# Kernel tuning notes

Measured on AMD Instinct MI355X. Metric: run time of the kernel, lower is better.

## Reference

```python
import jax, jax.numpy as jnp
import numpy as np

# config constants (from init_kwargs config['masking'])
MASK_RATIO = 0.15
SPAN_MIN = 5
SPAN_MAX = 20


def _generate_batch_masks(key, batch_size, seq_len):
    """Span-based random masking, exact-count adjusted. [B, S] bool."""
    target_masked = int(seq_len * MASK_RATIO)              # static
    avg_span = (SPAN_MIN + SPAN_MAX) / 2.0
    n_spans = max(1, int(target_masked / avg_span * 2))    # estimated_spans
    k_len, k_start, k_noise = jax.random.split(key, 3)

    span_lengths = jax.random.randint(k_len, (batch_size, n_spans), SPAN_MIN, SPAN_MAX + 1)
    starts = jax.random.randint(k_start, (batch_size, n_spans), 0, max(1, seq_len - SPAN_MIN))
    ends = jnp.minimum(starts + span_lengths, seq_len)

    # Span coverage via +1/-1 scatter + cumsum (equivalent to the per-span
    # boolean scatter loop in the torch code, fully on-device).
    b_idx = jnp.arange(batch_size)[:, None]
    delta = jnp.zeros((batch_size, seq_len + 1), jnp.int32)
    delta = delta.at[b_idx, starts].add(1).at[b_idx, ends].add(-1)
    coverage = jnp.cumsum(delta[:, :seq_len], axis=1) > 0   # [B, S] bool

    # Exact-count adjustment: equivalent to randomly removing excess masked
    # positions / randomly adding unmasked positions until count == target.
    # Masked positions get score in (1,2), unmasked in (0,1); top-k = keep a
    # random masked subset, fill remainder with random unmasked positions.
    noise = jax.random.uniform(k_noise, (batch_size, seq_len))
    score = coverage.astype(jnp.float32) + noise
    _, top_idx = jax.lax.top_k(score, target_masked)        # [B, target]
    masks = jnp.zeros((batch_size, seq_len), bool).at[b_idx, top_idx].set(True)
    return masks


def setup_inputs() -> dict:
    key = jax.random.key(0)
    k1, k2 = jax.random.split(key)
    features = jax.random.normal(k1, (128, 16384, 6), dtype=jnp.float32)
    mask_token = jax.random.normal(k2, (6,), dtype=jnp.float32) * 0.02
    return {"features": features, "mask_token": mask_token}


def reference(features, mask_token):
    B, S, F = features.shape
    key = jax.random.key(1234)  # plays the role of the module's torch.Generator seed
    masks = _generate_batch_masks(key, B, S)
    # _apply_valid_mask_vectorized: only mask non-NaN positions (channel 0)
    valid = ~jnp.isnan(features[:, :, 0])
    masks = masks & valid
    # apply_mask_to_features: replace masked positions with mask_token
    masked_features = jnp.where(masks[:, :, None], mask_token[None, None, :], features)
    return masked_features
```

## Files before the change

### kernel.cpp

```cpp
#include <hip/hip_runtime.h>
#include <stdint.h>

constexpr int NB = 128;
constexpr int SEQ = 16384;
constexpr int NF = 6;
constexpr int NSPANS = 393;
constexpr uint32_t TGT = 2457u;
constexpr int ROWF = SEQ * NF;
constexpr int ROWF4 = ROWF / 4;
constexpr int TOT4 = NB * ROWF4;

constexpr int FM_OFF = 0;
constexpr int FM_DW = NB * (SEQ / 32);
constexpr size_t WS_BYTES = (size_t)FM_DW * 4;

struct Keys {
  uint32_t klo0, klo1;
  uint32_t khi_s0, khi_s1;
  uint32_t klo_s0, klo_s1;
  uint32_t kn0, kn1;
};

__host__ __device__ inline void tf2x32(uint32_t k0, uint32_t k1,
                                       uint32_t x0, uint32_t x1,
                                       uint32_t& o0, uint32_t& o1) {
  uint32_t ks[3] = {k0, k1, k0 ^ k1 ^ 0x1BD11BDAu};
  uint32_t a = x0 + ks[0], b = x1 + ks[1];
  const uint32_t rot[2][4] = {{13u,15u,26u,6u},{17u,29u,16u,24u}};
#pragma unroll
  for (int i = 0; i < 5; ++i) {
    const uint32_t* r = rot[i & 1];
#pragma unroll
    for (int j = 0; j < 4; ++j) {
      a += b;
      b = (b << r[j]) | (b >> (32u - r[j]));
      b ^= a;
    }
    a += ks[(i + 1) % 3];
    b += ks[(i + 2) % 3] + (uint32_t)(i + 1);
  }
  o0 = a; o1 = b;
}

__device__ inline uint32_t rbits(uint32_t k0, uint32_t k1, uint32_t j) {
  uint32_t o0, o1;
  tf2x32(k0, k1, 0u, j, o0, o1);
  return o0 ^ o1;
}

__global__ __launch_bounds__(1024)
void maskgen_kernel(uint32_t* __restrict__ ws, Keys K) {
  __shared__ uint32_t hist[4096];
  __shared__ uint32_t cov[SEQ / 32];
  __shared__ uint32_t fm[SEQ / 32];
  __shared__ uint32_t wsum[16], ssum[16];
  __shared__ int tielist[256];
  __shared__ uint32_t sH, sA, sT, sN;
  __shared__ int tieCnt;

  const int t = threadIdx.x;
  const int lane = t & 63;
  const int wid = t >> 6;
  const uint32_t b = blockIdx.x;

  for (int i = t; i < 4096; i += 1024) hist[i] = 0u;
  if (t < SEQ / 32) cov[t] = 0u;
  if (t == 0) tieCnt = 0;
  __syncthreads();

  if (t < NSPANS) {
    uint32_t j = b * (uint32_t)NSPANS + (uint32_t)t;
    uint32_t lenb = rbits(K.klo0, K.klo1, j);
    uint32_t len = 5u + (lenb & 15u);
    uint32_t hb = rbits(K.khi_s0, K.khi_s1, j);
    uint32_t lb = rbits(K.klo_s0, K.klo_s1, j);
    const uint32_t span = 16379u;
    uint32_t start = ((hb % span) * 400u + (lb % span)) % span;
    uint32_t end = start + len; if (end > (uint32_t)SEQ) end = SEQ;
    uint32_t w0 = start >> 5, w1 = (end - 1u) >> 5;
    for (uint32_t w = w0; w <= w1; ++w) {
      uint32_t bs = (w == w0) ? (start & 31u) : 0u;
      uint32_t be = (w == w1) ? ((end - 1u) & 31u) : 31u;
      uint32_t n = be - bs + 1u;
      uint32_t m = (n >= 32u) ? 0xFFFFFFFFu : (((1u << n) - 1u) << bs);
      atomicOr(&cov[w], m);
    }
  }
  __syncthreads();

  const uint32_t jb = b << 14;
  uint32_t sr[16];
#pragma unroll
  for (int i = 0; i < 16; ++i) {
    int s = (i << 10) + t;
    uint32_t bits = rbits(K.kn0, K.kn1, jb + (uint32_t)s);
    uint32_t si = (bits >> 9) + (((cov[s >> 5] >> (s & 31)) & 1u) << 23);
    sr[i] = si;
    atomicAdd(&hist[si >> 12], 1u);
  }
  __syncthreads();

  {
    uint32_t mysum = 0;
#pragma unroll
    for (int i = 0; i < 4; ++i) mysum += hist[t * 4 + i];
    uint32_t v = mysum;
#pragma unroll
    for (int off = 1; off < 64; off <<= 1) {
      uint32_t n = __shfl_down(v, off, 64);
      if (lane + off < 64) v += n;
    }
    if (lane == 0) wsum[wid] = v;
    __syncthreads();
    if (t < 16) {
      uint32_t w = wsum[t];
#pragma unroll
      for (int off = 1; off < 16; off <<= 1) {
        uint32_t n = __shfl_down(w, off, 64);
        if (t + off < 16) w += n;
      }
      ssum[t] = w;
    }
    __syncthreads();
    uint32_t mine = v + (ssum[wid] - wsum[wid]);
    uint32_t above = mine - mysum;
    if (above < TGT && TGT <= mine) {
      uint32_t run = above;
      for (int hb = t * 4 + 3; hb >= t * 4; --hb) {
        uint32_t c = hist[hb];
        if (run + c >= TGT) { sH = (uint32_t)hb; sA = run; break; }
        run += c;
      }
    }
  }
  __syncthreads();
  uint32_t H = sH;
  uint32_t targetB = TGT - sA;

  for (int i = t; i < 4096; i += 1024) hist[i] = 0u;
  __syncthreads();

#pragma unroll
  for (int i = 0; i < 16; ++i) {
    uint32_t si = sr[i];
    if ((si >> 12) == H) atomicAdd(&hist[si & 4095u], 1u);
  }
  __syncthreads();
  {
    uint32_t mysum = 0;
#pragma unroll
    for (int i = 0; i < 4; ++i) mysum += hist[t * 4 + i];
    uint32_t v = mysum;
#pragma unroll
    for (int off = 1; off < 64; off <<= 1) {
      uint32_t n = __shfl_down(v, off, 64);
      if (lane + off < 64) v += n;
    }
    if (lane == 0) wsum[wid] = v;
    __syncthreads();
    if (t < 16) {
      uint32_t w = wsum[t];
#pragma unroll
      for (int off = 1; off < 16; off <<= 1) {
        uint32_t n = __shfl_down(w, off, 64);
        if (t + off < 16) w += n;
      }
      ssum[t] = w;
    }
    __syncthreads();
    uint32_t mine = v + (ssum[wid] - wsum[wid]);
    uint32_t above = mine - mysum;
    if (above < targetB && targetB <= mine) {
      uint32_t run = above;
      for (int lb = t * 4 + 3; lb >= t * 4; --lb) {
        uint32_t c = hist[lb];
        if (run + c >= targetB) {
          sT = (H << 12) | (uint32_t)lb;
          sN = targetB - run;
          break;
        }
        run += c;
      }
    }
  }
  __syncthreads();
  uint32_t T = sT, need = sN;

#pragma unroll
  for (int i = 0; i < 16; ++i) {
    int s = (i << 10) + t;
    uint32_t si = sr[i];
    unsigned long long bal = __ballot(si > T);
    if (si == T) {
      int idx = atomicAdd(&tieCnt, 1);
      if (idx < 256) tielist[idx] = s;
    }
    if (lane == 0)       fm[s >> 5] = (uint32_t)bal;
    else if (lane == 32) fm[s >> 5] = (uint32_t)(bal >> 32);
  }
  __syncthreads();
  int tc = tieCnt < 256 ? tieCnt : 256;
  if (t < tc) {
    int s = tielist[t];
    uint32_t rank = 0;
    for (int j = 0; j < tc; ++j) rank += (tielist[j] < s) ? 1u : 0u;
    if (rank < need) atomicOr(&fm[s >> 5], 1u << (s & 31));
  }
  __syncthreads();
  if (t < SEQ / 32) ws[FM_OFF + (b << 9) + t] = fm[t];
}

__global__ __launch_bounds__(256)
void apply3(const float* __restrict__ feat, const float* __restrict__ tok,
            const uint32_t* __restrict__ ws, float* __restrict__ out) {
  __shared__ float4 tile[768];
  const int t = threadIdx.x;
  const uint32_t n = blockIdx.x;
  const float4* f4 = (const float4*)feat + (size_t)n * 768;
  float4* o4 = (float4*)out + (size_t)n * 768;

  tile[t] = f4[t];
  tile[t + 256] = f4[t + 256];
  tile[t + 512] = f4[t + 512];
  uint32_t w = ws[FM_OFF + (n << 4) + (t >> 4)];
  float t0 = tok[0], t1 = tok[1], t2 = tok[2], t3 = tok[3], t4 = tok[4], t5 = tok[5];
  __syncthreads();

  float* lf = (float*)tile + t * 12;
  uint32_t bit0 = (uint32_t)(2 * t) & 31u;
  bool m0 = (w >> bit0) & 1u;
  bool m1 = (w >> (bit0 + 1u)) & 1u;
  m0 = m0 && !(lf[0] != lf[0]);
  m1 = m1 && !(lf[6] != lf[6]);
  if (m0) { lf[0] = t0; lf[1] = t1; lf[2] = t2; lf[3] = t3; lf[4] = t4; lf[5] = t5; }
  if (m1) { lf[6] = t0; lf[7] = t1; lf[8] = t2; lf[9] = t3; lf[10] = t4; lf[11] = t5; }
  __syncthreads();

  o4[t] = tile[t];
  o4[t + 256] = tile[t + 256];
  o4[t + 512] = tile[t + 512];
}


__device__ inline uint32_t score_int(const Keys& K, uint32_t b, int s,
                                     const uint32_t* cov) {
  uint32_t j = b * (uint32_t)SEQ + (uint32_t)s;
  uint32_t bits = rbits(K.kn0, K.kn1, j);
  return (bits >> 9) + (((cov[s >> 5] >> (s & 31)) & 1u) << 23);
}

__global__ __launch_bounds__(256)
void mask_kernel(const float* __restrict__ feat, const float* __restrict__ tok,
                 float* __restrict__ out, Keys K) {
  __shared__ uint32_t cov[SEQ / 32];
  __shared__ uint32_t fm[SEQ / 32];
  __shared__ uint32_t hist[4096];
  __shared__ uint32_t part[256];
  __shared__ uint32_t sH, sA, sT, sN;

  const int t = threadIdx.x;
  const uint32_t b = blockIdx.x;

  for (int i = t; i < 4096; i += 256) hist[i] = 0u;
  for (int i = t; i < SEQ / 32; i += 256) cov[i] = 0u;
  __syncthreads();

  for (int i = t; i < NSPANS; i += 256) {
    uint32_t j = b * (uint32_t)NSPANS + (uint32_t)i;
    uint32_t lenb = rbits(K.klo0, K.klo1, j);
    uint32_t len = 5u + (lenb & 15u);
    uint32_t hb = rbits(K.khi_s0, K.khi_s1, j);
    uint32_t lb = rbits(K.klo_s0, K.klo_s1, j);
    const uint32_t span = 16379u;
    uint32_t start = ((hb % span) * 400u + (lb % span)) % span;
    uint32_t end = start + len; if (end > (uint32_t)SEQ) end = SEQ;
    uint32_t w0 = start >> 5, w1 = (end - 1u) >> 5;
    for (uint32_t w = w0; w <= w1; ++w) {
      uint32_t bs = (w == w0) ? (start & 31u) : 0u;
      uint32_t be = (w == w1) ? ((end - 1u) & 31u) : 31u;
      uint32_t n = be - bs + 1u;
      uint32_t m = (n >= 32u) ? 0xFFFFFFFFu : (((1u << n) - 1u) << bs);
      atomicOr(&cov[w], m);
    }
  }
  __syncthreads();

  for (int q = 0; q < 64; ++q) {
    uint32_t si = score_int(K, b, t + (q << 8), cov);
    atomicAdd(&hist[si >> 12], 1u);
  }
  __syncthreads();
  {
    uint32_t sum = 0;
#pragma unroll
    for (int i = 0; i < 16; ++i) sum += hist[t * 16 + i];
    part[t] = sum;
    __syncthreads();
    for (int off = 1; off < 256; off <<= 1) {
      uint32_t v = (t + off < 256) ? part[t + off] : 0u;
      __syncthreads();
      part[t] += v;
      __syncthreads();
    }
    uint32_t above = (t < 255) ? part[t + 1] : 0u;
    uint32_t mine = part[t];
    if (above < TGT && TGT <= mine) {
      uint32_t run = above;
      for (int hb = t * 16 + 15; hb >= t * 16; --hb) {
        uint32_t c = hist[hb];
        if (run + c >= TGT) { sH = (uint32_t)hb; sA = run; break; }
        run += c;
      }
    }
  }
  __syncthreads();
  uint32_t H = sH;
  uint32_t targetB = TGT - sA;

  for (int i = t; i < 4096; i += 256) hist[i] = 0u;
  __syncthreads();
  for (int q = 0; q < 64; ++q) {
    uint32_t si = score_int(K, b, t + (q << 8), cov);
    if ((si >> 12) == H) atomicAdd(&hist[si & 4095u], 1u);
  }
  __syncthreads();
  {
    uint32_t sum = 0;
#pragma unroll
    for (int i = 0; i < 16; ++i) sum += hist[t * 16 + i];
    part[t] = sum;
    __syncthreads();
    for (int off = 1; off < 256; off <<= 1) {
      uint32_t v = (t + off < 256) ? part[t + off] : 0u;
      __syncthreads();
      part[t] += v;
      __syncthreads();
    }
    uint32_t above = (t < 255) ? part[t + 1] : 0u;
    uint32_t mine = part[t];
    if (above < targetB && targetB <= mine) {
      uint32_t run = above;
      for (int lb = t * 16 + 15; lb >= t * 16; --lb) {
        uint32_t c = hist[lb];
        if (run + c >= targetB) { sT = (H << 12) | (uint32_t)lb; sN = targetB - run; break; }
        run += c;
      }
    }
  }
  __syncthreads();
  uint32_t T = sT, need = sN;

  const float* rowf = feat + (size_t)b * ROWF;
  {
    int base = t << 6;
    uint32_t cnt = 0;
    for (int i = 0; i < 64; ++i) cnt += (score_int(K, b, base + i, cov) == T) ? 1u : 0u;
    part[t] = cnt;
    __syncthreads();
    for (int off = 1; off < 256; off <<= 1) {
      uint32_t v = (t >= off) ? part[t - off] : 0u;
      __syncthreads();
      part[t] += v;
      __syncthreads();
    }
    uint32_t r = part[t] - cnt;
    uint32_t w0 = 0, w1 = 0;
    for (int i = 0; i < 64; ++i) {
      int s = base + i;
      uint32_t si = score_int(K, b, s, cov);
      bool tie = (si == T);
      bool a = (si > T) || (tie && r < need);
      r += tie ? 1u : 0u;
      float f0 = rowf[s * 6];
      a = a && !(f0 != f0);
      if (i < 32) w0 |= ((uint32_t)a) << i;
      else        w1 |= ((uint32_t)a) << (i - 32);
    }
    fm[2 * t] = w0;
    fm[2 * t + 1] = w1;
  }
  __syncthreads();

  float tk[NF];
#pragma unroll
  for (int c = 0; c < NF; ++c) tk[c] = tok[c];
  float* rowo = out + (size_t)b * ROWF;
  const float4* rf4 = (const float4*)rowf;
  float4* ro4 = (float4*)rowo;
  for (int q = t; q < ROWF4; q += 256) {
    float4 v = rf4[q];
    float vv[4] = {v.x, v.y, v.z, v.w};
    int e = q * 4;
#pragma unroll
    for (int k = 0; k < 4; ++k) {
      int ee = e + k;
      int p = ee / 6;
      int c = ee - p * 6;
      if ((fm[p >> 5] >> (p & 31)) & 1u) vv[k] = tk[c];
    }
    ro4[q] = make_float4(vv[0], vv[1], vv[2], vv[3]);
  }
}

extern "C" void kernel_launch(void* const* d_in, const int* in_sizes, int n_in,
                              void* d_out, int out_size, void* d_ws, size_t ws_size,
                              hipStream_t stream) {
  const float* feat = (const float*)d_in[0];
  const float* tok = (const float*)d_in[1];
  float* out = (float*)d_out;

  uint32_t klen0, klen1, kst0, kst1, kn0, kn1;
  tf2x32(0u, 1234u, 0u, 0u, klen0, klen1);
  tf2x32(0u, 1234u, 0u, 1u, kst0, kst1);
  tf2x32(0u, 1234u, 0u, 2u, kn0, kn1);
  uint32_t lh0, lh1, ll0, ll1;
  tf2x32(klen0, klen1, 0u, 0u, lh0, lh1);
  tf2x32(klen0, klen1, 0u, 1u, ll0, ll1);
  (void)lh0; (void)lh1;
  uint32_t sh0, sh1, sl0, sl1;
  tf2x32(kst0, kst1, 0u, 0u, sh0, sh1);
  tf2x32(kst0, kst1, 0u, 1u, sl0, sl1);
  Keys K{ ll0, ll1, sh0, sh1, sl0, sl1, kn0, kn1 };

  if (ws_size >= WS_BYTES) {
    uint32_t* ws = (uint32_t*)d_ws;
    hipLaunchKernelGGL(maskgen_kernel, dim3(NB), dim3(1024), 0, stream, ws, K);
    hipLaunchKernelGGL(apply3, dim3(TOT4 / 768), dim3(256), 0, stream,
                       feat, tok, ws, out);
  } else {
    hipLaunchKernelGGL(mask_kernel, dim3(NB), dim3(256), 0, stream, feat, tok, out, K);
  }
}
```

Measured before the change: 112.3 us.

## Overlap bulk feature copy with mask generation and scatter-fix masked rows

The mask-generation kernel is launched with extra blocks that copy the whole feature tensor to the output, so the bulk copy runs concurrently with the compute-bound RNG/top-k blocks. A second sparse fixup kernel then walks only the set mask bits and overwrites those positions with the mask token after a NaN check. This hides mask generation latency behind the memory-bound copy, at the cost of the copy blocks sharing a 1024-thread, large-LDS block shape and a second pass of scattered writes to the output.

```diff
diff --git a/kernel.cpp b/kernel.cpp
--- a/kernel.cpp
+++ b/kernel.cpp
@@ -9,6 +9,7 @@
 constexpr int ROWF = SEQ * NF;
 constexpr int ROWF4 = ROWF / 4;
 constexpr int TOT4 = NB * ROWF4;
+constexpr int COPY_BLOCKS = TOT4 / 3072;
 
 constexpr int FM_OFF = 0;
 constexpr int FM_DW = NB * (SEQ / 32);
@@ -49,7 +50,8 @@
 }
 
 __global__ __launch_bounds__(1024)
-void maskgen_kernel(uint32_t* __restrict__ ws, Keys K) {
+void fused_kernel(const float* __restrict__ feat, float* __restrict__ out,
+                  uint32_t* __restrict__ ws, Keys K) {
   __shared__ uint32_t hist[4096];
   __shared__ uint32_t cov[SEQ / 32];
   __shared__ uint32_t fm[SEQ / 32];
@@ -59,6 +61,17 @@
   __shared__ int tieCnt;
 
   const int t = threadIdx.x;
+
+  if (blockIdx.x >= (unsigned)NB) {
+    const uint32_t n = blockIdx.x - NB;
+    const float4* f4 = (const float4*)feat + (size_t)n * 3072;
+    float4* o4 = (float4*)out + (size_t)n * 3072;
+    o4[t] = f4[t];
+    o4[t + 1024] = f4[t + 1024];
+    o4[t + 2048] = f4[t + 2048];
+    return;
+  }
+
   const int lane = t & 63;
   const int wid = t >> 6;
   const uint32_t b = blockIdx.x;
@@ -211,34 +224,23 @@
 }
 
 __global__ __launch_bounds__(256)
-void apply3(const float* __restrict__ feat, const float* __restrict__ tok,
-            const uint32_t* __restrict__ ws, float* __restrict__ out) {
-  __shared__ float4 tile[768];
-  const int t = threadIdx.x;
-  const uint32_t n = blockIdx.x;
-  const float4* f4 = (const float4*)feat + (size_t)n * 768;
-  float4* o4 = (float4*)out + (size_t)n * 768;
-
-  tile[t] = f4[t];
-  tile[t + 256] = f4[t + 256];
-  tile[t + 512] = f4[t + 512];
-  uint32_t w = ws[FM_OFF + (n << 4) + (t >> 4)];
+void fixup_kernel(const float* __restrict__ feat, const float* __restrict__ tok,
+                  const uint32_t* __restrict__ ws, float* __restrict__ out) {
+  int g = blockIdx.x * 256 + threadIdx.x;
+  uint32_t w = ws[FM_OFF + g];
+  if (!w) return;
   float t0 = tok[0], t1 = tok[1], t2 = tok[2], t3 = tok[3], t4 = tok[4], t5 = tok[5];
-  __syncthreads();
-
-  float* lf = (float*)tile + t * 12;
-  uint32_t bit0 = (uint32_t)(2 * t) & 31u;
-  bool m0 = (w >> bit0) & 1u;
-  bool m1 = (w >> (bit0 + 1u)) & 1u;
-  m0 = m0 && !(lf[0] != lf[0]);
-  m1 = m1 && !(lf[6] != lf[6]);
-  if (m0) { lf[0] = t0; lf[1] = t1; lf[2] = t2; lf[3] = t3; lf[4] = t4; lf[5] = t5; }
-  if (m1) { lf[6] = t0; lf[7] = t1; lf[8] = t2; lf[9] = t3; lf[10] = t4; lf[11] = t5; }
-  __syncthreads();
-
-  o4[t] = tile[t];
-  o4[t + 256] = tile[t + 256];
-  o4[t + 512] = tile[t + 512];
+  size_t basePos = (size_t)g * 32;
+  while (w) {
+    int bit = __ffs(w) - 1;
+    w &= w - 1u;
+    size_t p = basePos + (size_t)bit;
+    float c0 = feat[p * 6];
+    if (!(c0 != c0)) {
+      float* o = out + p * 6;
+      o[0] = t0; o[1] = t1; o[2] = t2; o[3] = t3; o[4] = t4; o[5] = t5;
+    }
+  }
 }
 
 
@@ -424,8 +426,9 @@
 
   if (ws_size >= WS_BYTES) {
     uint32_t* ws = (uint32_t*)d_ws;
-    hipLaunchKernelGGL(maskgen_kernel, dim3(NB), dim3(1024), 0, stream, ws, K);
-    hipLaunchKernelGGL(apply3, dim3(TOT4 / 768), dim3(256), 0, stream,
+    hipLaunchKernelGGL(fused_kernel, dim3(NB + COPY_BLOCKS), dim3(1024), 0, stream,
+                       feat, out, ws, K);
+    hipLaunchKernelGGL(fixup_kernel, dim3(FM_DW / 256), dim3(256), 0, stream,
                        feat, tok, ws, out);
   } else {
     hipLaunchKernelGGL(mask_kernel, dim3(NB), dim3(256), 0, stream, feat, tok, out, K);
```

After: 111.5 us. No clear change (-0.7%).
